# Optimization experiments

Hardware: AMD Instinct MI355X
Metric: run time of the kernel (lower is better)

The kernel has to match this reference:

```python
import jax, jax.numpy as jnp
import numpy as np

H = 512  # hidden size

def gru_cell(x, h, Wih, Whh, bih, bhh):
    # PyTorch GRU cell: gates ordered [r, z, n]
    gi = x @ Wih.T + bih          # (B, 3H)
    gh = h @ Whh.T + bhh          # (B, 3H)
    ir, iz, inn = gi[:, :H], gi[:, H:2*H], gi[:, 2*H:]
    hr, hz, hn = gh[:, :H], gh[:, H:2*H], gh[:, 2*H:]
    r = jax.nn.sigmoid(ir + hr)
    z = jax.nn.sigmoid(iz + hz)
    n = jnp.tanh(inn + r * hn)
    return (1.0 - z) * n + z * h

def setup_inputs() -> dict:
    key = jax.random.key(0)
    ks = jax.random.split(key, 12)
    S, B, V, E, OUT = 400, 128, 50000, 300, 2
    s = 0.05
    return {
        "X": jax.random.randint(ks[0], (S, B), 0, V, dtype=jnp.int32),
        "emb": jax.random.normal(ks[1], (V, E), jnp.float32),
        "Wih0": jax.random.normal(ks[2], (2, 3*H, E), jnp.float32) * s,
        "Whh0": jax.random.normal(ks[3], (2, 3*H, H), jnp.float32) * s,
        "bih0": jax.random.normal(ks[4], (2, 3*H), jnp.float32) * s,
        "bhh0": jax.random.normal(ks[5], (2, 3*H), jnp.float32) * s,
        "Wih1": jax.random.normal(ks[6], (2, 3*H, 2*H), jnp.float32) * s,
        "Whh1": jax.random.normal(ks[7], (2, 3*H, H), jnp.float32) * s,
        "bih1": jax.random.normal(ks[8], (2, 3*H), jnp.float32) * s,
        "bhh1": jax.random.normal(ks[9], (2, 3*H), jnp.float32) * s,
        "Ws": jax.random.normal(ks[10], (OUT, 2*H), jnp.float32) * s,
        "bs": jax.random.normal(ks[11], (OUT,), jnp.float32) * s,
    }

def reference(X, emb, Wih0, Whh0, bih0, bhh0, Wih1, Whh1, bih1, bhh1, Ws, bs):
    # NOTE: the original torch code feeds the bidirectional GRU one timestep
    # at a time while threading ht, so the 'reverse' direction ALSO runs
    # left-to-right (with its own weights). We reproduce exactly that.
    S, B = X.shape
    embedded = emb[X]  # (S, B, E)
    h0 = jnp.zeros((B, H), embedded.dtype)

    def step(carry, xt):
        h0f, h0b, h1f, h1b = carry
        h0f = gru_cell(xt, h0f, Wih0[0], Whh0[0], bih0[0], bhh0[0])
        h0b = gru_cell(xt, h0b, Wih0[1], Whh0[1], bih0[1], bhh0[1])
        y0 = jnp.concatenate([h0f, h0b], axis=-1)  # (B, 2H)
        h1f = gru_cell(y0, h1f, Wih1[0], Whh1[0], bih1[0], bhh1[0])
        h1b = gru_cell(y0, h1b, Wih1[1], Whh1[1], bih1[1], bhh1[1])
        return (h1f := h1f, h0b, h1f, h1b) if False else ((h0f, h0b, h1f, h1b), None)

    (h0f, h0b, h1f, h1b), _ = jax.lax.scan(step, (h0, h0, h0, h0), embedded)
    yt = jnp.concatenate([h1f, h1b], axis=-1)  # (B, 2H) last-step output
    logits = yt @ Ws.T + bs
    return jax.nn.log_softmax(logits, axis=1)
```

## Files before the change

kernel.cpp:

```cpp
#include <hip/hip_runtime.h>


typedef unsigned int u32;
typedef unsigned short u16;
typedef __attribute__((ext_vector_type(8))) _Float16 f16x8;
typedef __attribute__((ext_vector_type(4))) float f32x4;
typedef __attribute__((ext_vector_type(16))) float f32x16;
typedef __attribute__((ext_vector_type(4))) u32 u32x4;

#define AS1 __attribute__((address_space(1)))
#define AS3 __attribute__((address_space(3)))

__device__ __forceinline__ void gl_lds16(const void* g, void* l) {
  __builtin_amdgcn_global_load_lds((AS1 void*)g, (AS3 void*)l, 16, 0, 0);
}
__device__ __forceinline__ u16 f2h(float f) {
  _Float16 h = (_Float16)f;
  return __builtin_bit_cast(u16, h);
}
__device__ __forceinline__ u32 pack2(float a, float b) {
  return (u32)f2h(a) | ((u32)f2h(b) << 16);
}
__device__ __forceinline__ float sigm(float x) {
  x = fminf(fmaxf(x, -30.f), 30.f);
  return 1.f / (1.f + __expf(-x));
}
__device__ __forceinline__ float tanh_(float x) {
  x = fminf(fmaxf(x, -15.f), 15.f);
  float e = __expf(2.f * x);
  return (e - 1.f) / (e + 1.f);
}
__device__ __forceinline__ f32x16 mfma32(f16x8 a, f16x8 b, f32x16 c) {
  return __builtin_amdgcn_mfma_f32_32x32x16_f16(a, b, c, 0, 0, 0);
}
__device__ __forceinline__ f16x8 load_cc(const u16* sbase, u32 voff) {
  f16x8 r;
  asm volatile("global_load_dwordx4 %0, %1, %2 sc0 sc1"
               : "=v"(r) : "v"(voff), "s"(sbase) : "memory");
  return r;
}
__device__ __forceinline__ void store_cc16(u16* sbase, u32 voff, u32 val) {
  asm volatile("global_store_short %0, %1, %2 sc0 sc1"
               :: "v"(voff), "v"(val), "s"(sbase) : "memory");
}
__device__ __forceinline__ void wait_vm0() {
  asm volatile("s_waitcnt vmcnt(0)" ::: "memory");
}

__global__ __launch_bounds__(256) void pack_wih(const float* __restrict__ W,
                                                u16* __restrict__ out, int K, int Kp, int total) {
  int idx = blockIdx.x * 256 + threadIdx.x;
  if (idx >= total) return;
  int n = idx / Kp, k = idx - n * Kp;
  out[idx] = (k < K) ? f2h(W[(size_t)n * K + k]) : (u16)0;
}

__global__ __launch_bounds__(256) void pack_whh(const float* __restrict__ W,
                                                u16* __restrict__ out) {
  int idx = blockIdx.x * 256 + threadIdx.x;
  int l = idx & 63;
  int kt = (idx >> 6) & 31;
  int rest = idx >> 11;
  int g = rest % 3, dc = rest / 3;
  int d = dc >> 4, c = dc & 15;
  int row = g * 512 + c * 32 + (l & 31);
  int k0 = kt * 16 + (l >> 5) * 8;
  const float* src = W + ((size_t)d * 1536 + row) * 512 + k0;
  u32* o = (u32*)(out + (size_t)idx * 8);
#pragma unroll
  for (int e2 = 0; e2 < 4; ++e2) o[e2] = pack2(src[2 * e2], src[2 * e2 + 1]);
}

__global__ __launch_bounds__(256) void pack_bias(const float* __restrict__ bih,
                                                 const float* __restrict__ bhh,
                                                 float* __restrict__ out) {
  int idx = blockIdx.x * 256 + threadIdx.x;
  int j = idx & 511;
  int slot = (idx >> 9) & 3;
  int d = idx >> 11;
  float v;
  if (slot == 0) v = bih[d * 1536 + j] + bhh[d * 1536 + j];
  else if (slot == 1) v = bih[d * 1536 + 512 + j] + bhh[d * 1536 + 512 + j];
  else if (slot == 2) v = bih[d * 1536 + 1024 + j];
  else v = bhh[d * 1536 + 1024 + j];
  out[idx] = v;
}

__global__ __launch_bounds__(256) void gather_emb(const int* __restrict__ X,
                                                  const float* __restrict__ emb,
                                                  u32* __restrict__ out, int t0, int total) {
  int idx = blockIdx.x * 256 + threadIdx.x;
  if (idx >= total) return;
  int r = idx / 160, kp = idx - r * 160;
  int k = kp * 2;
  int tok = X[t0 * 128 + r];
  float v0 = (k < 300) ? emb[(size_t)tok * 300 + k] : 0.f;
  float v1 = (k < 299) ? emb[(size_t)tok * 300 + k + 1] : 0.f;
  out[idx] = pack2(v0, v1);
}

__global__ __launch_bounds__(256) void gemm_f16(const u16* __restrict__ A,
                                                const u16* __restrict__ B,
                                                u16* __restrict__ giP, int K) {
  __shared__ u16 As[4096];
  __shared__ u16 Bs[4096];
  const int tid = threadIdx.x;
  const int w = tid >> 6, l = tid & 63;
  const long m0 = (long)blockIdx.y << 7;
  const long n0 = (long)blockIdx.x << 7;
  const int wm = w >> 1, wn = w & 1;
  f32x4 acc[4][4] = {};

  const int srow = w * 16 + (l >> 2);
  const int scol = (l & 3) * 8;
  const u16* ga = A + (m0 + srow) * K + scol;
  const u16* gb = B + (n0 + srow) * K + scol;
  u16* lA = &As[w * 512];
  u16* lB = &Bs[w * 512];

  for (int k0 = 0; k0 < K; k0 += 32) {
    gl_lds16(ga + k0, lA);
    gl_lds16(ga + 64 * K + k0, lA + 2048);
    gl_lds16(gb + k0, lB);
    gl_lds16(gb + 64 * K + k0, lB + 2048);
    __syncthreads();
    f16x8 af[4], bf[4];
#pragma unroll
    for (int mi = 0; mi < 4; ++mi)
      af[mi] = *(const f16x8*)&As[(wm * 64 + mi * 16 + (l & 15)) * 32 + ((l >> 4) & 3) * 8];
#pragma unroll
    for (int ni = 0; ni < 4; ++ni)
      bf[ni] = *(const f16x8*)&Bs[(wn * 64 + ni * 16 + (l & 15)) * 32 + ((l >> 4) & 3) * 8];
#pragma unroll
    for (int mi = 0; mi < 4; ++mi)
#pragma unroll
      for (int ni = 0; ni < 4; ++ni)
        acc[mi][ni] = __builtin_amdgcn_mfma_f32_16x16x32_f16(af[mi], bf[ni], acc[mi][ni], 0, 0, 0);
    __syncthreads();
  }
  const int crow = wm * 64 + ((l >> 4) << 2);
  const int ccol = wn * 64 + (l & 15);
#pragma unroll
  for (int mi = 0; mi < 4; ++mi)
#pragma unroll
    for (int ni = 0; ni < 4; ++ni)
#pragma unroll
      for (int i = 0; i < 4; ++i) {
        int grow = (int)m0 + crow + mi * 16 + i;
        int col = (int)n0 + ccol + ni * 16;
        int t_rel = grow >> 7, b = grow & 127;
        int dd = (col >= 1536) ? 1 : 0;
        int cc2 = col - dd * 1536;
        int g = cc2 >> 9, ch = (cc2 >> 5) & 15, jj = cc2 & 31;
        int wt = b >> 5, reg = (b & 3) | (((b >> 3) & 3) << 2), l5 = (b >> 2) & 1;
        int lt = jj | (l5 << 5);
        int s = g * 16 + reg, n2 = s >> 3, e = s & 7;
        size_t idx = (((((size_t)t_rel * 2 + dd) * 16 + ch) * 4 + wt) * 6 + n2) * 512 + lt * 8 + e;
        giP[idx] = f2h(acc[mi][ni][i]);
      }
}

__global__ __launch_bounds__(256, 1) void gru_layer(const u16* __restrict__ gi,
                                                    const u16* __restrict__ WhhP,
                                                    const float* __restrict__ biasP,
                                                    float* __restrict__ hf,
                                                    u16* __restrict__ hp,
                                                    u16* __restrict__ y0,
                                                    u32* __restrict__ flags,
                                                    int t0, int TC) {
  const int bid = blockIdx.x;
  const int d = bid >> 4, c = bid & 15;
  const int tid = threadIdx.x;
  const int w = tid >> 6, l = tid & 63;

  __shared__ u16 Wl[49152];

  {
    const u32x4* src = (const u32x4*)(WhhP + (size_t)(d * 16 + c) * 49152);
    u32x4* dst = (u32x4*)Wl;
#pragma unroll
    for (int i = 0; i < 24; ++i) dst[i * 256 + tid] = src[i * 256 + tid];
  }

  const int jcol = c * 32 + (l & 31);
  const float bsr = biasP[(d * 4 + 0) * 512 + jcol];
  const float bsz = biasP[(d * 4 + 1) * 512 + jcol];
  const float bin = biasP[(d * 4 + 2) * 512 + jcol];
  const float bhn = biasP[(d * 4 + 3) * 512 + jcol];

  const int l5 = l >> 5;
  float hreg[16];
#pragma unroll
  for (int r = 0; r < 16; ++r) {
    int row = (r & 3) + 8 * (r >> 2) + 4 * l5;
    hreg[r] = hf[((size_t)d * 128 + w * 32 + row) * 512 + jcol];
  }
  __syncthreads();

  f16x8 giv[6];
  {
    const u16* gp = gi + (((size_t)(0 * 2 + d) * 16 + c) * 4 + w) * 3072 + l * 8;
#pragma unroll
    for (int n2 = 0; n2 < 6; ++n2) giv[n2] = *(const f16x8*)(gp + n2 * 512);
  }

  const u32 aoffbase = (u32)((d * 4 + w) * 32768 + l * 16);
  const int ktj = jcol >> 4;
  const int lb5 = ((l >> 3) & 1) << 5;
  const int ej = l & 7;
  const u32 foff = (u32)((l & 15) * 4);

  for (int t = t0; t < t0 + TC; ++t) {
    {
      const u32* fb = flags + (size_t)(d * 4 + (t & 3)) * 16;
      for (;;) {
        u32 v;
        asm volatile("global_load_dword %0, %1, %2 sc0 sc1\n\ts_waitcnt vmcnt(0)"
                     : "=v"(v) : "v"(foff), "s"(fb) : "memory");
        if (__all((int)(v >= (u32)t))) break;
      }
    }

    const u16* hrb = hp + (size_t)(t & 3) * 131072;
    f16x8 a[32];
#pragma unroll
    for (int kt = 0; kt < 32; ++kt) a[kt] = load_cc(hrb, aoffbase + (u32)kt * 1024u);

    f32x16 accR = {}, accZ = {}, accN = {};
#pragma unroll
    for (int g4 = 0; g4 < 8; ++g4) {
      switch (g4) {
        case 0: asm volatile("s_waitcnt vmcnt(28)" ::: "memory"); break;
        case 1: asm volatile("s_waitcnt vmcnt(24)" ::: "memory"); break;
        case 2: asm volatile("s_waitcnt vmcnt(20)" ::: "memory"); break;
        case 3: asm volatile("s_waitcnt vmcnt(16)" ::: "memory"); break;
        case 4: asm volatile("s_waitcnt vmcnt(12)" ::: "memory"); break;
        case 5: asm volatile("s_waitcnt vmcnt(8)" ::: "memory"); break;
        case 6: asm volatile("s_waitcnt vmcnt(4)" ::: "memory"); break;
        default: asm volatile("s_waitcnt vmcnt(0)" ::: "memory"); break;
      }
      __builtin_amdgcn_sched_barrier(0);
#pragma unroll
      for (int kk = 0; kk < 4; ++kk) {
        int kt = g4 * 4 + kk;
        f16x8 b0 = *(const f16x8*)&Wl[(0 * 32 + kt) * 512 + l * 8];
        f16x8 b1 = *(const f16x8*)&Wl[(1 * 32 + kt) * 512 + l * 8];
        f16x8 b2 = *(const f16x8*)&Wl[(2 * 32 + kt) * 512 + l * 8];
        accR = mfma32(a[kt], b0, accR);
        accZ = mfma32(a[kt], b1, accZ);
        accN = mfma32(a[kt], b2, accN);
      }
    }

    u16* hwb = hp + (size_t)((t + 1) & 3) * 131072;
#pragma unroll
    for (int r = 0; r < 16; ++r) {
      float gr = (float)giv[r >> 3][r & 7];
      float gz = (float)giv[2 + (r >> 3)][r & 7];
      float gn = (float)giv[4 + (r >> 3)][r & 7];
      float rr = sigm(gr + accR[r] + bsr);
      float zz = sigm(gz + accZ[r] + bsz);
      float nn = tanh_(gn + bin + rr * (accN[r] + bhn));
      float h = (1.f - zz) * nn + zz * hreg[r];
      hreg[r] = h;
      int row = (r & 3) + 8 * (r >> 2) + 4 * l5;
      u32 voff = (u32)(((((d * 4 + w) * 32 + ktj) * 64 + (row | lb5)) * 8 + ej) * 2);
      store_cc16(hwb, voff, (u32)f2h(h));
      if (y0) {
        int b = w * 32 + row;
        y0[((size_t)t * 128 + b) * 1024 + d * 512 + jcol] = f2h(h);
      }
    }

    {
      int rel = t + 1 - t0;
      if (rel >= TC) rel = TC - 1;
      const u16* gp = gi + (((size_t)rel * 2 + d) * 16 + c) * 4 * 3072 + (size_t)w * 3072 + l * 8;
#pragma unroll
      for (int n2 = 0; n2 < 6; ++n2) giv[n2] = *(const f16x8*)(gp + n2 * 512);
    }

    asm volatile("s_waitcnt vmcnt(0)" ::: "memory");
    __syncthreads();
    if (tid == 0) {
      u32* fw = flags + (size_t)(d * 4 + ((t + 1) & 3)) * 16 + c;
      u32 val = (u32)(t + 1);
      asm volatile("global_store_dword %0, %1, %2 sc0 sc1"
                   :: "v"(0u), "v"(val), "s"(fw) : "memory");
    }
  }

#pragma unroll
  for (int r = 0; r < 16; ++r) {
    int row = (r & 3) + 8 * (r >> 2) + 4 * l5;
    hf[((size_t)d * 128 + w * 32 + row) * 512 + jcol] = hreg[r];
  }
  wait_vm0();
}

__global__ __launch_bounds__(128) void classify(const float* __restrict__ hf,
                                                const float* __restrict__ Ws,
                                                const float* __restrict__ bs,
                                                float* __restrict__ out) {
  int b = threadIdx.x;
  float l0 = bs[0], l1 = bs[1];
#pragma unroll 8
  for (int j = 0; j < 512; ++j) {
    float v = hf[b * 512 + j];
    l0 = fmaf(v, Ws[j], l0);
    l1 = fmaf(v, Ws[1024 + j], l1);
  }
#pragma unroll 8
  for (int j = 0; j < 512; ++j) {
    float v = hf[(128 + b) * 512 + j];
    l0 = fmaf(v, Ws[512 + j], l0);
    l1 = fmaf(v, Ws[1536 + j], l1);
  }
  float m = fmaxf(l0, l1);
  float lse = m + __logf(__expf(l0 - m) + __expf(l1 - m));
  out[b * 2] = l0 - lse;
  out[b * 2 + 1] = l1 - lse;
}

extern "C" void kernel_launch(void* const* d_in, const int* in_sizes, int n_in,
                              void* d_out, int out_size, void* d_ws, size_t ws_size,
                              hipStream_t stream) {
  const int* X = (const int*)d_in[0];
  const float* emb = (const float*)d_in[1];
  const float* Wih0 = (const float*)d_in[2];
  const float* Whh0 = (const float*)d_in[3];
  const float* bih0 = (const float*)d_in[4];
  const float* bhh0 = (const float*)d_in[5];
  const float* Wih1 = (const float*)d_in[6];
  const float* Whh1 = (const float*)d_in[7];
  const float* bih1 = (const float*)d_in[8];
  const float* bhh1 = (const float*)d_in[9];
  const float* Ws = (const float*)d_in[10];
  const float* bs = (const float*)d_in[11];
  float* out = (float*)d_out;

  const int S = 400, B = 128;
  auto need = [&](int nc) -> size_t {
    size_t TC = (size_t)S / nc, R = TC * B;
    size_t sz = 0;
    sz += R * 3072 * 2;
    sz += (size_t)S * B * 1024 * 2;
    sz += R * 320 * 2;
    sz += (size_t)3072 * 320 * 2;
    sz += (size_t)3072 * 1024 * 2;
    sz += 2 * (size_t)1572864 * 2;
    sz += 2 * (size_t)4096 * 4;
    sz += 2 * (size_t)131072 * 4;
    sz += 2 * (size_t)524288 * 2;
    sz += 65536;
    return sz;
  };
  int nc = 16;
  if (need(1) <= ws_size) nc = 1;
  else if (need(2) <= ws_size) nc = 2;
  else if (need(4) <= ws_size) nc = 4;
  else if (need(8) <= ws_size) nc = 8;
  const int TC = S / nc;
  const size_t R = (size_t)TC * B;

  char* p = (char*)d_ws;
  auto alloc = [&](size_t bytes) {
    char* q = p;
    p += (bytes + 255) & ~(size_t)255;
    return q;
  };
  u16* giPack = (u16*)alloc(R * 3072 * 2);
  u16* y0 = (u16*)alloc((size_t)S * B * 1024 * 2);
  u16* embC = (u16*)alloc(R * 320 * 2);
  u16* B0p = (u16*)alloc((size_t)3072 * 320 * 2);
  u16* B1p = (u16*)alloc((size_t)3072 * 1024 * 2);
  u16* WhhP0 = (u16*)alloc((size_t)1572864 * 2);
  u16* WhhP1 = (u16*)alloc((size_t)1572864 * 2);
  float* biasP0 = (float*)alloc(4096 * 4);
  float* biasP1 = (float*)alloc(4096 * 4);
  float* hf0 = (float*)alloc(131072 * 4);
  float* hf1 = (float*)alloc(131072 * 4);
  u16* hp0 = (u16*)alloc(524288 * 2);
  u16* hp1 = (u16*)alloc(524288 * 2);
  u32* flags0 = (u32*)alloc(1024);
  u32* flags1 = (u32*)alloc(1024);

  hipMemsetAsync(hf0, 0, 131072 * 4, stream);
  hipMemsetAsync(hf1, 0, 131072 * 4, stream);
  hipMemsetAsync(hp0, 0, 524288 * 2, stream);
  hipMemsetAsync(hp1, 0, 524288 * 2, stream);
  hipMemsetAsync(flags0, 0, 1024, stream);
  hipMemsetAsync(flags1, 0, 1024, stream);

  pack_wih<<<3840, 256, 0, stream>>>(Wih0, B0p, 300, 320, 3072 * 320);
  pack_wih<<<12288, 256, 0, stream>>>(Wih1, B1p, 1024, 1024, 3072 * 1024);
  pack_whh<<<768, 256, 0, stream>>>(Whh0, WhhP0);
  pack_whh<<<768, 256, 0, stream>>>(Whh1, WhhP1);
  pack_bias<<<16, 256, 0, stream>>>(bih0, bhh0, biasP0);
  pack_bias<<<16, 256, 0, stream>>>(bih1, bhh1, biasP1);

  dim3 gg(24, (unsigned)(R / 128));
  for (int cix = 0; cix < nc; ++cix) {
    int t0 = cix * TC;
    int total = (int)(R * 160);
    gather_emb<<<(total + 255) / 256, 256, 0, stream>>>(X, emb, (u32*)embC, t0, total);
    gemm_f16<<<gg, 256, 0, stream>>>(embC, B0p, giPack, 320);
    gru_layer<<<32, 256, 0, stream>>>(giPack, WhhP0, biasP0, hf0, hp0, y0, flags0, t0, TC);
  }
  for (int cix = 0; cix < nc; ++cix) {
    int t0 = cix * TC;
    gemm_f16<<<gg, 256, 0, stream>>>(y0 + (size_t)t0 * 128 * 1024, B1p, giPack, 1024);
    gru_layer<<<32, 256, 0, stream>>>(giPack, WhhP1, biasP1, hf1, hp1, (u16*)nullptr, flags1, t0, TC);
  }
  classify<<<1, 128, 0, stream>>>(hf1, Ws, bs, out);
}
```

Measured before the change: 6.710 ms.

## Transpose GRU MFMA output, vectorize hidden-state stores, per-wave flags, fold biases into GEMM

The recurrent MFMA operands are swapped so each lane holds one batch row across consecutive hidden columns. Packed fp16 hidden state can then be exchanged with a cross-half shuffle and written as 128-bit coherent stores instead of per-element short stores, and y0 is stored in a pre-packed layout that a new layer-1 GEMM reads directly. The block-wide barrier before signalling is replaced by per-wave flags, each written after a partial vmcnt wait. The r/z/in biases are folded into the input GEMM epilogue. This cuts store traffic and sync cost on the serial critical path, but adds more flags to poll and requires careful memory ordering.

```diff
diff --git a/kernel.cpp b/kernel.cpp
--- a/kernel.cpp
+++ b/kernel.cpp
@@ -39,8 +39,12 @@
                : "=v"(r) : "v"(voff), "s"(sbase) : "memory");
   return r;
 }
-__device__ __forceinline__ void store_cc16(u16* sbase, u32 voff, u32 val) {
-  asm volatile("global_store_short %0, %1, %2 sc0 sc1"
+__device__ __forceinline__ void store_cc128(u16* sbase, u32 voff, u32x4 v) {
+  asm volatile("global_store_dwordx4 %0, %1, %2 sc0 sc1"
+               :: "v"(voff), "v"(v), "s"(sbase) : "memory");
+}
+__device__ __forceinline__ void store_cc32(u32* sbase, u32 voff, u32 val) {
+  asm volatile("global_store_dword %0, %1, %2 sc0 sc1"
                :: "v"(voff), "v"(val), "s"(sbase) : "memory");
 }
 __device__ __forceinline__ void wait_vm0() {
@@ -71,19 +75,24 @@
   for (int e2 = 0; e2 < 4; ++e2) o[e2] = pack2(src[2 * e2], src[2 * e2 + 1]);
 }
 
-__global__ __launch_bounds__(256) void pack_bias(const float* __restrict__ bih,
-                                                 const float* __restrict__ bhh,
-                                                 float* __restrict__ out) {
+__global__ __launch_bounds__(256) void pack_biasg(const float* __restrict__ bih,
+                                                  const float* __restrict__ bhh,
+                                                  float* __restrict__ biasG,
+                                                  float* __restrict__ bhnG) {
   int idx = blockIdx.x * 256 + threadIdx.x;
-  int j = idx & 511;
-  int slot = (idx >> 9) & 3;
-  int d = idx >> 11;
-  float v;
-  if (slot == 0) v = bih[d * 1536 + j] + bhh[d * 1536 + j];
-  else if (slot == 1) v = bih[d * 1536 + 512 + j] + bhh[d * 1536 + 512 + j];
-  else if (slot == 2) v = bih[d * 1536 + 1024 + j];
-  else v = bhh[d * 1536 + 1024 + j];
-  out[idx] = v;
+  if (idx < 3072) {
+    int d = idx / 1536, rest = idx - d * 1536;
+    int g = rest >> 9, j = rest & 511;
+    float v;
+    if (g == 0) v = bih[d * 1536 + j] + bhh[d * 1536 + j];
+    else if (g == 1) v = bih[d * 1536 + 512 + j] + bhh[d * 1536 + 512 + j];
+    else v = bih[d * 1536 + 1024 + j];
+    biasG[idx] = v;
+  } else {
+    int k = idx - 3072;
+    int d = k >> 9, j = k & 511;
+    bhnG[k] = bhh[d * 1536 + 1024 + j];
+  }
 }
 
 __global__ __launch_bounds__(256) void gather_emb(const int* __restrict__ X,
@@ -99,8 +108,21 @@
   out[idx] = pack2(v0, v1);
 }
 
+__device__ __forceinline__ size_t gip_idx(int t_rel, int grow_b, int col) {
+  int dd = (col >= 1536) ? 1 : 0;
+  int cc2 = col - dd * 1536;
+  int g = cc2 >> 9, ch = (cc2 >> 5) & 15, jj = cc2 & 31;
+  int wA = grow_b >> 5, lb = grow_b & 31;
+  int l5 = (jj >> 2) & 1;
+  int lt = lb | (l5 << 5);
+  int r = (jj & 3) | ((jj >> 3) << 2);
+  int n2 = g * 2 + (r >> 3), e = r & 7;
+  return ((((size_t)t_rel * 2 + dd) * 16 + ch) * 4 + wA) * 3072 + (size_t)n2 * 512 + lt * 8 + e;
+}
+
 __global__ __launch_bounds__(256) void gemm_f16(const u16* __restrict__ A,
                                                 const u16* __restrict__ B,
+                                                const float* __restrict__ biasG,
                                                 u16* __restrict__ giP, int K) {
   __shared__ u16 As[4096];
   __shared__ u16 Bs[4096];
@@ -148,21 +170,70 @@
       for (int i = 0; i < 4; ++i) {
         int grow = (int)m0 + crow + mi * 16 + i;
         int col = (int)n0 + ccol + ni * 16;
-        int t_rel = grow >> 7, b = grow & 127;
-        int dd = (col >= 1536) ? 1 : 0;
-        int cc2 = col - dd * 1536;
-        int g = cc2 >> 9, ch = (cc2 >> 5) & 15, jj = cc2 & 31;
-        int wt = b >> 5, reg = (b & 3) | (((b >> 3) & 3) << 2), l5 = (b >> 2) & 1;
-        int lt = jj | (l5 << 5);
-        int s = g * 16 + reg, n2 = s >> 3, e = s & 7;
-        size_t idx = (((((size_t)t_rel * 2 + dd) * 16 + ch) * 4 + wt) * 6 + n2) * 512 + lt * 8 + e;
-        giP[idx] = f2h(acc[mi][ni][i]);
+        giP[gip_idx(grow >> 7, grow & 127, col)] = f2h(acc[mi][ni][i] + biasG[col]);
+      }
+}
+
+__global__ __launch_bounds__(256) void gemm_l1(const u16* __restrict__ y0P,
+                                               const u16* __restrict__ B,
+                                               const float* __restrict__ biasG,
+                                               u16* __restrict__ giP, int t0) {
+  __shared__ u16 Bs[4096];
+  const int tid = threadIdx.x;
+  const int w = tid >> 6, l = tid & 63;
+  const long m0 = (long)blockIdx.y << 7;
+  const long n0 = (long)blockIdx.x << 7;
+  const int wm = w >> 1, wn = w & 1;
+  const int K = 1024;
+  f32x4 acc[4][4] = {};
+
+  const int srow = w * 16 + (l >> 2);
+  const int scol = (l & 3) * 8;
+  const u16* gb = B + (n0 + srow) * K + scol;
+  u16* lB = &Bs[w * 512];
+
+  for (int k0 = 0; k0 < K; k0 += 32) {
+    gl_lds16(gb + k0, lB);
+    gl_lds16(gb + 64 * K + k0, lB + 2048);
+    __syncthreads();
+    f16x8 af[4], bf[4];
+    const int k = k0 + ((l >> 4) & 3) * 8;
+    const int dk = k >> 9, ktg = (k >> 4) & 31, l5A = (k >> 3) & 1;
+#pragma unroll
+    for (int mi = 0; mi < 4; ++mi) {
+      int row = (int)m0 + wm * 64 + mi * 16 + (l & 15);
+      int t = t0 + (row >> 7), b = row & 127;
+      int wA = b >> 5, l31 = b & 31;
+      size_t idx = (((((size_t)t * 2 + dk) * 32 + ktg) * 4 + wA) * 64 + (l31 | (l5A << 5))) * 8;
+      af[mi] = *(const f16x8*)(y0P + idx);
+    }
+#pragma unroll
+    for (int ni = 0; ni < 4; ++ni)
+      bf[ni] = *(const f16x8*)&Bs[(wn * 64 + ni * 16 + (l & 15)) * 32 + ((l >> 4) & 3) * 8];
+#pragma unroll
+    for (int mi = 0; mi < 4; ++mi)
+#pragma unroll
+      for (int ni = 0; ni < 4; ++ni)
+        acc[mi][ni] = __builtin_amdgcn_mfma_f32_16x16x32_f16(af[mi], bf[ni], acc[mi][ni], 0, 0, 0);
+    __syncthreads();
+  }
+  const int crow = wm * 64 + ((l >> 4) << 2);
+  const int ccol = wn * 64 + (l & 15);
+#pragma unroll
+  for (int mi = 0; mi < 4; ++mi)
+#pragma unroll
+    for (int ni = 0; ni < 4; ++ni)
+#pragma unroll
+      for (int i = 0; i < 4; ++i) {
+        int grow = (int)m0 + crow + mi * 16 + i;
+        int col = (int)n0 + ccol + ni * 16;
+        giP[gip_idx(grow >> 7, grow & 127, col)] = f2h(acc[mi][ni][i] + biasG[col]);
       }
 }
 
 __global__ __launch_bounds__(256, 1) void gru_layer(const u16* __restrict__ gi,
                                                     const u16* __restrict__ WhhP,
-                                                    const float* __restrict__ biasP,
+                                                    const float* __restrict__ bhnG,
                                                     float* __restrict__ hf,
                                                     u16* __restrict__ hp,
                                                     u16* __restrict__ y0,
@@ -172,6 +243,7 @@
   const int d = bid >> 4, c = bid & 15;
   const int tid = threadIdx.x;
   const int w = tid >> 6, l = tid & 63;
+  const int l31 = l & 31, l5 = l >> 5;
 
   __shared__ u16 Wl[49152];
 
@@ -182,37 +254,29 @@
     for (int i = 0; i < 24; ++i) dst[i * 256 + tid] = src[i * 256 + tid];
   }
 
-  const int jcol = c * 32 + (l & 31);
-  const float bsr = biasP[(d * 4 + 0) * 512 + jcol];
-  const float bsz = biasP[(d * 4 + 1) * 512 + jcol];
-  const float bin = biasP[(d * 4 + 2) * 512 + jcol];
-  const float bhn = biasP[(d * 4 + 3) * 512 + jcol];
-
-  const int l5 = l >> 5;
-  float hreg[16];
+  float bhnv[16], hreg[16];
 #pragma unroll
   for (int r = 0; r < 16; ++r) {
-    int row = (r & 3) + 8 * (r >> 2) + 4 * l5;
-    hreg[r] = hf[((size_t)d * 128 + w * 32 + row) * 512 + jcol];
+    int col = c * 32 + (r & 3) + 8 * (r >> 2) + 4 * l5;
+    bhnv[r] = bhnG[d * 512 + col];
+    hreg[r] = hf[((size_t)d * 128 + w * 32 + l31) * 512 + col];
   }
   __syncthreads();
 
   f16x8 giv[6];
   {
-    const u16* gp = gi + (((size_t)(0 * 2 + d) * 16 + c) * 4 + w) * 3072 + l * 8;
+    const u16* gp = gi + (((size_t)d * 16 + c) * 4 + w) * 3072 + l * 8;
 #pragma unroll
     for (int n2 = 0; n2 < 6; ++n2) giv[n2] = *(const f16x8*)(gp + n2 * 512);
   }
+  wait_vm0();
 
   const u32 aoffbase = (u32)((d * 4 + w) * 32768 + l * 16);
-  const int ktj = jcol >> 4;
-  const int lb5 = ((l >> 3) & 1) << 5;
-  const int ej = l & 7;
-  const u32 foff = (u32)((l & 15) * 4);
+  const u32 foff = (u32)(l * 4);
 
   for (int t = t0; t < t0 + TC; ++t) {
     {
-      const u32* fb = flags + (size_t)(d * 4 + (t & 3)) * 16;
+      const u32* fb = flags + (size_t)(d * 4 + (t & 3)) * 64;
       for (;;) {
         u32 v;
         asm volatile("global_load_dword %0, %1, %2 sc0 sc1\n\ts_waitcnt vmcnt(0)"
@@ -246,54 +310,83 @@
         f16x8 b0 = *(const f16x8*)&Wl[(0 * 32 + kt) * 512 + l * 8];
         f16x8 b1 = *(const f16x8*)&Wl[(1 * 32 + kt) * 512 + l * 8];
         f16x8 b2 = *(const f16x8*)&Wl[(2 * 32 + kt) * 512 + l * 8];
-        accR = mfma32(a[kt], b0, accR);
-        accZ = mfma32(a[kt], b1, accZ);
-        accN = mfma32(a[kt], b2, accN);
-      }
-    }
-
-    u16* hwb = hp + (size_t)((t + 1) & 3) * 131072;
+        accR = mfma32(b0, a[kt], accR);
+        accZ = mfma32(b1, a[kt], accZ);
+        accN = mfma32(b2, a[kt], accN);
+      }
+    }
+
+    float hn[16];
 #pragma unroll
     for (int r = 0; r < 16; ++r) {
       float gr = (float)giv[r >> 3][r & 7];
       float gz = (float)giv[2 + (r >> 3)][r & 7];
       float gn = (float)giv[4 + (r >> 3)][r & 7];
-      float rr = sigm(gr + accR[r] + bsr);
-      float zz = sigm(gz + accZ[r] + bsz);
-      float nn = tanh_(gn + bin + rr * (accN[r] + bhn));
-      float h = (1.f - zz) * nn + zz * hreg[r];
-      hreg[r] = h;
-      int row = (r & 3) + 8 * (r >> 2) + 4 * l5;
-      u32 voff = (u32)(((((d * 4 + w) * 32 + ktj) * 64 + (row | lb5)) * 8 + ej) * 2);
-      store_cc16(hwb, voff, (u32)f2h(h));
+      float rr = sigm(gr + accR[r]);
+      float zz = sigm(gz + accZ[r]);
+      float nn = tanh_(gn + rr * (accN[r] + bhnv[r]));
+      hn[r] = (1.f - zz) * nn + zz * hreg[r];
+      hreg[r] = hn[r];
+    }
+
+    u32 Wpk[4][2];
+#pragma unroll
+    for (int a2 = 0; a2 < 4; ++a2)
+#pragma unroll
+      for (int p = 0; p < 2; ++p)
+        Wpk[a2][p] = pack2(hn[4 * a2 + 2 * p], hn[4 * a2 + 2 * p + 1]);
+    u32 X[2][2], S[2][2], Y[2][2];
+#pragma unroll
+    for (int kt = 0; kt < 2; ++kt)
+#pragma unroll
+      for (int p = 0; p < 2; ++p) {
+        X[kt][p] = l5 ? Wpk[2 * kt + 1][p] : Wpk[2 * kt][p];
+        S[kt][p] = l5 ? Wpk[2 * kt][p] : Wpk[2 * kt + 1][p];
+      }
+#pragma unroll
+    for (int kt = 0; kt < 2; ++kt)
+#pragma unroll
+      for (int p = 0; p < 2; ++p)
+        Y[kt][p] = (u32)__shfl_xor((int)S[kt][p], 32);
+
+    u16* hwb = hp + (size_t)((t + 1) & 3) * 131072;
+#pragma unroll
+    for (int kt = 0; kt < 2; ++kt) {
+      u32x4 wv;
+      wv[0] = l5 ? Y[kt][0] : X[kt][0];
+      wv[1] = l5 ? Y[kt][1] : X[kt][1];
+      wv[2] = l5 ? X[kt][0] : Y[kt][0];
+      wv[3] = l5 ? X[kt][1] : Y[kt][1];
+      u32 hoff = (u32)((((d * 4 + w) * 32 + (c * 2 + kt)) * 64 + l) * 16);
+      store_cc128(hwb, hoff, wv);
       if (y0) {
-        int b = w * 32 + row;
-        y0[((size_t)t * 128 + b) * 1024 + d * 512 + jcol] = f2h(h);
-      }
-    }
-
+        size_t yi = ((((size_t)t * 2 + d) * 32 + (c * 2 + kt)) * 4 + w) * 512 + (size_t)l * 8;
+        *(u32x4*)(y0 + yi) = wv;
+      }
+    }
+
+    f16x8 gt[6];
     {
       int rel = t + 1 - t0;
       if (rel >= TC) rel = TC - 1;
-      const u16* gp = gi + (((size_t)rel * 2 + d) * 16 + c) * 4 * 3072 + (size_t)w * 3072 + l * 8;
-#pragma unroll
-      for (int n2 = 0; n2 < 6; ++n2) giv[n2] = *(const f16x8*)(gp + n2 * 512);
-    }
-
-    asm volatile("s_waitcnt vmcnt(0)" ::: "memory");
-    __syncthreads();
-    if (tid == 0) {
-      u32* fw = flags + (size_t)(d * 4 + ((t + 1) & 3)) * 16 + c;
-      u32 val = (u32)(t + 1);
-      asm volatile("global_store_dword %0, %1, %2 sc0 sc1"
-                   :: "v"(0u), "v"(val), "s"(fw) : "memory");
-    }
+      const u16* gp = gi + (((size_t)rel * 2 + d) * 16 + c) * 12288 + (size_t)w * 3072 + l * 8;
+#pragma unroll
+      for (int n2 = 0; n2 < 6; ++n2) gt[n2] = *(const f16x8*)(gp + n2 * 512);
+    }
+
+    asm volatile("s_waitcnt vmcnt(6)" ::: "memory");
+    if (l == 0) {
+      u32* fw = flags + (size_t)(d * 4 + ((t + 1) & 3)) * 64;
+      store_cc32(fw, (u32)((c * 4 + w) * 4), (u32)(t + 1));
+    }
+#pragma unroll
+    for (int n2 = 0; n2 < 6; ++n2) giv[n2] = gt[n2];
   }
 
 #pragma unroll
   for (int r = 0; r < 16; ++r) {
-    int row = (r & 3) + 8 * (r >> 2) + 4 * l5;
-    hf[((size_t)d * 128 + w * 32 + row) * 512 + jcol] = hreg[r];
+    int col = c * 32 + (r & 3) + 8 * (r >> 2) + 4 * l5;
+    hf[((size_t)d * 128 + w * 32 + l31) * 512 + col] = hreg[r];
   }
   wait_vm0();
 }
@@ -370,47 +463,49 @@
     return q;
   };
   u16* giPack = (u16*)alloc(R * 3072 * 2);
-  u16* y0 = (u16*)alloc((size_t)S * B * 1024 * 2);
+  u16* y0P = (u16*)alloc((size_t)S * B * 1024 * 2);
   u16* embC = (u16*)alloc(R * 320 * 2);
   u16* B0p = (u16*)alloc((size_t)3072 * 320 * 2);
   u16* B1p = (u16*)alloc((size_t)3072 * 1024 * 2);
   u16* WhhP0 = (u16*)alloc((size_t)1572864 * 2);
   u16* WhhP1 = (u16*)alloc((size_t)1572864 * 2);
-  float* biasP0 = (float*)alloc(4096 * 4);
-  float* biasP1 = (float*)alloc(4096 * 4);
+  float* biasG0 = (float*)alloc(3072 * 4);
+  float* bhnG0 = (float*)alloc(1024 * 4);
+  float* biasG1 = (float*)alloc(3072 * 4);
+  float* bhnG1 = (float*)alloc(1024 * 4);
   float* hf0 = (float*)alloc(131072 * 4);
   float* hf1 = (float*)alloc(131072 * 4);
   u16* hp0 = (u16*)alloc(524288 * 2);
   u16* hp1 = (u16*)alloc(524288 * 2);
-  u32* flags0 = (u32*)alloc(1024);
-  u32* flags1 = (u32*)alloc(1024);
+  u32* flags0 = (u32*)alloc(4096);
+  u32* flags1 = (u32*)alloc(4096);
 
   hipMemsetAsync(hf0, 0, 131072 * 4, stream);
   hipMemsetAsync(hf1, 0, 131072 * 4, stream);
   hipMemsetAsync(hp0, 0, 524288 * 2, stream);
   hipMemsetAsync(hp1, 0, 524288 * 2, stream);
-  hipMemsetAsync(flags0, 0, 1024, stream);
-  hipMemsetAsync(flags1, 0, 1024, stream);
+  hipMemsetAsync(flags0, 0, 4096, stream);
+  hipMemsetAsync(flags1, 0, 4096, stream);
 
   pack_wih<<<3840, 256, 0, stream>>>(Wih0, B0p, 300, 320, 3072 * 320);
   pack_wih<<<12288, 256, 0, stream>>>(Wih1, B1p, 1024, 1024, 3072 * 1024);
   pack_whh<<<768, 256, 0, stream>>>(Whh0, WhhP0);
   pack_whh<<<768, 256, 0, stream>>>(Whh1, WhhP1);
-  pack_bias<<<16, 256, 0, stream>>>(bih0, bhh0, biasP0);
-  pack_bias<<<16, 256, 0, stream>>>(bih1, bhh1, biasP1);
+  pack_biasg<<<16, 256, 0, stream>>>(bih0, bhh0, biasG0, bhnG0);
+  pack_biasg<<<16, 256, 0, stream>>>(bih1, bhh1, biasG1, bhnG1);
 
   dim3 gg(24, (unsigned)(R / 128));
   for (int cix = 0; cix < nc; ++cix) {
     int t0 = cix * TC;
     int total = (int)(R * 160);
     gather_emb<<<(total + 255) / 256, 256, 0, stream>>>(X, emb, (u32*)embC, t0, total);
-    gemm_f16<<<gg, 256, 0, stream>>>(embC, B0p, giPack, 320);
-    gru_layer<<<32, 256, 0, stream>>>(giPack, WhhP0, biasP0, hf0, hp0, y0, flags0, t0, TC);
+    gemm_f16<<<gg, 256, 0, stream>>>(embC, B0p, biasG0, giPack, 320);
+    gru_layer<<<32, 256, 0, stream>>>(giPack, WhhP0, bhnG0, hf0, hp0, y0P, flags0, t0, TC);
   }
   for (int cix = 0; cix < nc; ++cix) {
     int t0 = cix * TC;
-    gemm_f16<<<gg, 256, 0, stream>>>(y0 + (size_t)t0 * 128 * 1024, B1p, giPack, 1024);
-    gru_layer<<<32, 256, 0, stream>>>(giPack, WhhP1, biasP1, hf1, hp1, (u16*)nullptr, flags1, t0, TC);
+    gemm_l1<<<gg, 256, 0, stream>>>(y0P, B1p, biasG1, giPack, t0);
+    gru_layer<<<32, 256, 0, stream>>>(giPack, WhhP1, bhnG1, hf1, hp1, (u16*)nullptr, flags1, t0, TC);
   }
   classify<<<1, 128, 0, stream>>>(hf1, Ws, bs, out);
 }
```

Result: slower. 7.831 ms (+16.7%).
